# Kernel tuning notes

Hardware: AMD Instinct MI355X
Metric: run time of the kernel (lower is better)

Reference implementation:

```python
import jax, jax.numpy as jnp
import numpy as np

NUM_EXPERTS = 8
TOP_K = 2


def setup_inputs() -> dict:
    key = jax.random.key(0)
    ks = jax.random.split(key, 6)
    D, H, E = 1024, 4096, NUM_EXPERTS
    B, S = 4, 2048
    s = 0.02
    return {
        "x": jax.random.normal(ks[0], (B, S, D), jnp.float32),
        "scale_embeddings": jax.random.normal(ks[1], (10, D), jnp.float32) * s,
        "router_w": jax.random.normal(ks[2], (E, D), jnp.float32) * s,
        "router_b": jnp.zeros((E,), jnp.float32),
        "fc1_w": jax.random.normal(ks[3], (E, H, D), jnp.float32) * s,
        "fc1_b": jnp.zeros((E, H), jnp.float32),
        "fc2_w": jax.random.normal(ks[4], (E, D, H), jnp.float32) * s,
        "fc2_b": jnp.zeros((E, D), jnp.float32),
        "scale_idx": 3,
    }


def reference(x, scale_embeddings, router_w, router_b, fc1_w, fc1_b, fc2_w, fc2_b, scale_idx):
    B, S, D = x.shape
    T = B * S
    # Scale-aware router (eval mode: no jitter, temperature=1.0).
    xs = x + scale_embeddings[scale_idx][None, None, :]
    logits = jnp.einsum('bsd,ed->bse', xs, router_w) + router_b  # [B,S,E]
    top_w, top_idx = jax.lax.top_k(logits, TOP_K)                 # [B,S,K]
    top_w = jax.nn.softmax(top_w, axis=-1)

    # Dense per-expert FFN (tanh-approx GELU), then gather top-k expert outputs.
    xf = x.reshape(T, D)
    outs = []
    for e in range(NUM_EXPERTS):
        h = jax.nn.gelu(xf @ fc1_w[e].T + fc1_b[e], approximate=True)  # [T,H]
        outs.append(h @ fc2_w[e].T + fc2_b[e])                          # [T,D]
    all_out = jnp.stack(outs)                                           # [E,T,D]

    idx_f = top_idx.reshape(T, TOP_K)
    w_f = top_w.reshape(T, TOP_K)
    gathered = all_out[idx_f, jnp.arange(T)[:, None]]  # [T,K,D]
    out = (gathered * w_f[..., None]).sum(axis=1)      # [T,D]
    return out.reshape(B, S, D)
```

## Files before the change

### kernel.cpp

```cpp
#include <hip/hip_runtime.h>
#include <math.h>

#define TTOK 8192
#define DDIM 1024
#define HDIM 4096
#define NEXP 8
#define NASSIGN (TTOK * 2)

typedef float f32x4 __attribute__((ext_vector_type(4)));
typedef short s16x8 __attribute__((ext_vector_type(8)));

__device__ __forceinline__ unsigned short f2bf(float f) {
  union { float f; unsigned int u; } v; v.f = f;
  unsigned int u = v.u;
  u += 0x7FFFu + ((u >> 16) & 1u);
  return (unsigned short)(u >> 16);
}

__device__ __forceinline__ float gelu_fast(float x) {
  float u = 0.7978845608028654f * x * (1.0f + 0.044715f * x * x);
  return x / (1.0f + __expf(-2.0f * u));
}

__global__ void cvt_bf16_k(const float* __restrict__ w1, unsigned short* __restrict__ w1b,
                           const float* __restrict__ w2, unsigned short* __restrict__ w2b,
                           int n8) {
  int i = blockIdx.x * blockDim.x + threadIdx.x;
  const float* src; unsigned short* dst;
  if (i < n8) { src = w1; dst = w1b; } else { src = w2; dst = w2b; i -= n8; }
#pragma unroll
  for (int c = 0; c < 2; ++c) {
    float4 v = ((const float4*)src)[i * 2 + c];
    ushort4 o;
    o.x = f2bf(v.x); o.y = f2bf(v.y); o.z = f2bf(v.z); o.w = f2bf(v.w);
    ((ushort4*)dst)[i * 2 + c] = o;
  }
}

__global__ void router_k(const float* __restrict__ x, const float* __restrict__ se,
                         const int* __restrict__ sidx, const float* __restrict__ rw,
                         const float* __restrict__ rb,
                         int* __restrict__ e0, int* __restrict__ e1,
                         float* __restrict__ w0, float* __restrict__ w1,
                         int* __restrict__ counts) {
  int t = blockIdx.x * 4 + (threadIdx.x >> 6);
  int lane = threadIdx.x & 63;
  const float4* xp = (const float4*)(x + (size_t)t * DDIM) + lane * 4;
  const float4* sp = (const float4*)(se + (size_t)sidx[0] * DDIM) + lane * 4;
  float xs[16];
#pragma unroll
  for (int c = 0; c < 4; ++c) {
    float4 a = xp[c], b = sp[c];
    xs[c * 4 + 0] = a.x + b.x; xs[c * 4 + 1] = a.y + b.y;
    xs[c * 4 + 2] = a.z + b.z; xs[c * 4 + 3] = a.w + b.w;
  }
  double acc[NEXP];
#pragma unroll
  for (int e = 0; e < NEXP; ++e) acc[e] = 0.0;
#pragma unroll
  for (int e = 0; e < NEXP; ++e) {
    const float4* wp = (const float4*)(rw + (size_t)e * DDIM) + lane * 4;
#pragma unroll
    for (int c = 0; c < 4; ++c) {
      float4 wv = wp[c];
      acc[e] += (double)xs[c * 4 + 0] * wv.x + (double)xs[c * 4 + 1] * wv.y +
                (double)xs[c * 4 + 2] * wv.z + (double)xs[c * 4 + 3] * wv.w;
    }
  }
#pragma unroll
  for (int e = 0; e < NEXP; ++e) {
#pragma unroll
    for (int m = 32; m >= 1; m >>= 1) acc[e] += __shfl_xor(acc[e], m, 64);
  }
  if (lane == 0) {
    float lg[NEXP];
    for (int e = 0; e < NEXP; ++e) lg[e] = (float)acc[e] + rb[e];
    int i0 = 0; float l0 = lg[0];
    for (int e = 1; e < NEXP; ++e) if (lg[e] > l0) { l0 = lg[e]; i0 = e; }
    int i1 = -1; float l1 = -1e30f;
    for (int e = 0; e < NEXP; ++e) if (e != i0 && lg[e] > l1) { l1 = lg[e]; i1 = e; }
    float z = expf(l1 - l0);
    float p0 = 1.0f / (1.0f + z);
    e0[t] = i0; e1[t] = i1; w0[t] = p0; w1[t] = 1.0f - p0;
    atomicAdd(&counts[i0], 1);
    atomicAdd(&counts[i1], 1);
  }
}

__global__ void scan_k(const int* __restrict__ counts, int* __restrict__ offsets,
                       int* __restrict__ cursors, int4* __restrict__ tileT,
                       int* __restrict__ ntiles) {
  if (threadIdx.x == 0 && blockIdx.x == 0) {
    int s = 0;
    for (int e = 0; e < NEXP; ++e) { offsets[e] = s; cursors[e] = s; s += counts[e]; }
    offsets[NEXP] = s;
    int nt = 0;
    for (int e = 0; e < NEXP; ++e)
      for (int m0 = offsets[e]; m0 < offsets[e + 1]; m0 += 128)
        tileT[nt++] = make_int4(m0, offsets[e + 1], e, 0);
    ntiles[0] = nt;
  }
}

__global__ void scatter_k(const int* __restrict__ e0, const int* __restrict__ e1,
                          const float* __restrict__ w0, const float* __restrict__ w1,
                          int* __restrict__ cursors, int* __restrict__ buckets,
                          float* __restrict__ wts, int* __restrict__ s0,
                          int* __restrict__ s1) {
  int t = blockIdx.x * blockDim.x + threadIdx.x;
  if (t >= TTOK) return;
  int a = e0[t];
  int p = atomicAdd(&cursors[a], 1);
  buckets[p] = t; wts[p] = w0[t]; s0[t] = p;
  a = e1[t];
  p = atomicAdd(&cursors[a], 1);
  buckets[p] = t; wts[p] = w1[t]; s1[t] = p;
}

__global__ void gather_k(const float* __restrict__ x, const int* __restrict__ buckets,
                         unsigned short* __restrict__ Xg) {
  int r = blockIdx.x;
  int t = buckets[r];
  int i = threadIdx.x;
  float4 v = ((const float4*)(x + (size_t)t * DDIM))[i];
  ushort4 o;
  o.x = f2bf(v.x); o.y = f2bf(v.y); o.z = f2bf(v.z); o.w = f2bf(v.w);
  ((ushort4*)(Xg + (size_t)r * DDIM))[i] = o;
}

template <int KD, int ND, int EPI>
__global__ __launch_bounds__(256) void moe_gemm_k(
    const unsigned short* __restrict__ A,
    const unsigned short* __restrict__ W,
    const float* __restrict__ bias,
    const int4* __restrict__ tileT, const int* __restrict__ ntiles,
    unsigned short* __restrict__ Hout, float* __restrict__ Yout) {
  constexpr int NT = ND / 128;
  constexpr int G = NT / 8;
  __shared__ unsigned short As[128 * 64];
  __shared__ unsigned short Bs[128 * 64];

  const int tid = threadIdx.x;
  const int lane = tid & 63;
  const int w = tid >> 6;
  const int q = lane >> 4;
  const int c16 = lane & 15;
  const int cx = lane & 7;
  const int wrow = (w >> 1) * 64;
  const int wcol = (w & 1) * 64;
  const int srow = w * 8 + (lane >> 3);
  const int swz = (lane & 7) ^ (lane >> 3);

  const int xcd = blockIdx.x & 7;
  const int lid = blockIdx.x >> 3;
  const int bound = ntiles[0] * G;

  for (int idx = lid; idx < bound; idx += 256) {
    const int mt = idx / G;
    const int nb = xcd * G + (idx - mt * G);
    const int4 tl = tileT[mt];
    const int m0 = tl.x, row1 = tl.y, e = tl.z;
    const int n0 = nb * 128;
    const unsigned short* We = W + (size_t)e * ND * KD;

    const unsigned short* aptr[4];
    const unsigned short* bptr[4];
#pragma unroll
    for (int i = 0; i < 4; ++i) {
      int ar = m0 + i * 32 + srow;
      if (ar > row1 - 1) ar = row1 - 1;
      aptr[i] = A + (size_t)ar * KD + swz * 8;
      bptr[i] = We + (size_t)(n0 + i * 32 + srow) * KD + swz * 8;
    }

    f32x4 acc[4][4];
#pragma unroll
    for (int i = 0; i < 4; ++i)
#pragma unroll
      for (int j = 0; j < 4; ++j) acc[i][j] = {0.f, 0.f, 0.f, 0.f};

    for (int kt = 0; kt < KD / 64; ++kt) {
      const int k0 = kt * 64;
      __syncthreads();
#pragma unroll
      for (int i = 0; i < 4; ++i)
        __builtin_amdgcn_global_load_lds(
            (const __attribute__((address_space(1))) void*)(aptr[i] + k0),
            (__attribute__((address_space(3))) void*)(As + (i * 32 + w * 8) * 64),
            16, 0, 0);
#pragma unroll
      for (int i = 0; i < 4; ++i)
        __builtin_amdgcn_global_load_lds(
            (const __attribute__((address_space(1))) void*)(bptr[i] + k0),
            (__attribute__((address_space(3))) void*)(Bs + (i * 32 + w * 8) * 64),
            16, 0, 0);
      __syncthreads();
#pragma unroll
      for (int ks = 0; ks < 2; ++ks) {
        s16x8 af[4], bfr[4];
#pragma unroll
        for (int i = 0; i < 4; ++i)
          af[i] = *((const s16x8*)(As + (wrow + i * 16 + c16) * 64 +
                                   (((ks * 4 + q) ^ cx) * 8)));
#pragma unroll
        for (int j = 0; j < 4; ++j)
          bfr[j] = *((const s16x8*)(Bs + (wcol + j * 16 + c16) * 64 +
                                    (((ks * 4 + q) ^ cx) * 8)));
#pragma unroll
        for (int i = 0; i < 4; ++i)
#pragma unroll
          for (int j = 0; j < 4; ++j)
            acc[i][j] = __builtin_amdgcn_mfma_f32_16x16x32_bf16(af[i], bfr[j], acc[i][j], 0, 0, 0);
      }
    }

    float bj[4];
#pragma unroll
    for (int j = 0; j < 4; ++j)
      bj[j] = bias[(size_t)e * ND + n0 + wcol + j * 16 + c16];
#pragma unroll
    for (int i = 0; i < 4; ++i) {
#pragma unroll
      for (int r = 0; r < 4; ++r) {
        const int m = m0 + wrow + i * 16 + q * 4 + r;
        if (m < row1) {
          if (EPI == 0) {
#pragma unroll
            for (int j = 0; j < 4; ++j) {
              const int n = n0 + wcol + j * 16 + c16;
              Hout[(size_t)m * ND + n] = f2bf(gelu_fast(acc[i][j][r] + bj[j]));
            }
          } else {
#pragma unroll
            for (int j = 0; j < 4; ++j) {
              const int n = n0 + wcol + j * 16 + c16;
              Yout[(size_t)m * ND + n] = acc[i][j][r] + bj[j];
            }
          }
        }
      }
    }
  }
}

__global__ void combine_k(const float* __restrict__ Yr, const int* __restrict__ s0,
                          const int* __restrict__ s1, const float* __restrict__ wts,
                          float* __restrict__ out) {
  int t = blockIdx.x;
  int i = threadIdx.x;
  int a = s0[t], b = s1[t];
  float wa = wts[a], wb = wts[b];
  float4 va = ((const float4*)(Yr + (size_t)a * DDIM))[i];
  float4 vb = ((const float4*)(Yr + (size_t)b * DDIM))[i];
  float4 o;
  o.x = wa * va.x + wb * vb.x;
  o.y = wa * va.y + wb * vb.y;
  o.z = wa * va.z + wb * vb.z;
  o.w = wa * va.w + wb * vb.w;
  ((float4*)(out + (size_t)t * DDIM))[i] = o;
}

extern "C" void kernel_launch(void* const* d_in, const int* in_sizes, int n_in,
                              void* d_out, int out_size, void* d_ws, size_t ws_size,
                              hipStream_t stream) {
  const float* x  = (const float*)d_in[0];
  const float* se = (const float*)d_in[1];
  const float* rw = (const float*)d_in[2];
  const float* rb = (const float*)d_in[3];
  const float* w1 = (const float*)d_in[4];
  const float* b1 = (const float*)d_in[5];
  const float* w2 = (const float*)d_in[6];
  const float* b2 = (const float*)d_in[7];
  const int* sidx = (const int*)d_in[8];
  float* out = (float*)d_out;

  char* ws = (char*)d_ws;
  size_t off = 0;
  unsigned short* w1b = (unsigned short*)(ws + off); off += (size_t)NEXP * HDIM * DDIM * 2;
  unsigned short* w2b = (unsigned short*)(ws + off); off += (size_t)NEXP * DDIM * HDIM * 2;
  unsigned short* Xg  = (unsigned short*)(ws + off); off += (size_t)NASSIGN * DDIM * 2;
  unsigned short* Hb  = (unsigned short*)(ws + off); off += (size_t)NASSIGN * HDIM * 2;
  float* Yr = (float*)w1b;
  int*   counts  = (int*)(ws + off); off += 64;
  int*   offsets = (int*)(ws + off); off += 64;
  int*   cursors = (int*)(ws + off); off += 64;
  int*   ntiles  = (int*)(ws + off); off += 64;
  int*   e0  = (int*)(ws + off);   off += (size_t)TTOK * 4;
  int*   e1  = (int*)(ws + off);   off += (size_t)TTOK * 4;
  float* tw0 = (float*)(ws + off); off += (size_t)TTOK * 4;
  float* tw1 = (float*)(ws + off); off += (size_t)TTOK * 4;
  int*   s0  = (int*)(ws + off);   off += (size_t)TTOK * 4;
  int*   s1  = (int*)(ws + off);   off += (size_t)TTOK * 4;
  int*   buckets = (int*)(ws + off); off += (size_t)NASSIGN * 4;
  float* wts = (float*)(ws + off);   off += (size_t)NASSIGN * 4;
  int4*  tileT = (int4*)(ws + off);  off += 256 * 16;

  hipMemsetAsync(counts, 0, 64, stream);

  const int n8 = NEXP * HDIM * DDIM / 8;
  cvt_bf16_k<<<2 * n8 / 256, 256, 0, stream>>>(w1, w1b, w2, w2b, n8);
  router_k<<<TTOK / 4, 256, 0, stream>>>(x, se, sidx, rw, rb, e0, e1, tw0, tw1, counts);
  scan_k<<<1, 64, 0, stream>>>(counts, offsets, cursors, tileT, ntiles);
  scatter_k<<<TTOK / 256, 256, 0, stream>>>(e0, e1, tw0, tw1, cursors, buckets, wts, s0, s1);
  gather_k<<<NASSIGN, 256, 0, stream>>>(x, buckets, Xg);

  moe_gemm_k<DDIM, HDIM, 0><<<2048, 256, 0, stream>>>(Xg, w1b, b1, tileT, ntiles, Hb, Yr);
  moe_gemm_k<HDIM, DDIM, 1><<<2048, 256, 0, stream>>>(Hb, w2b, b2, tileT, ntiles, Hb, Yr);
  combine_k<<<TTOK, 256, 0, stream>>>(Yr, s0, s1, wts, out);
}
```

Measured before the change: 1.145 ms.

## Double-buffer MoE GEMM LDS tiles and fuse scatter with token gather

The GEMM main loop switches from single-buffered 64-wide K tiles, with two barriers per step, to double-buffered 32-wide K tiles. The next stage's global-to-LDS loads are issued before the current stage is computed, with one barrier per step. The scatter and gather kernels are merged into one per-token kernel that converts x once and writes it to both assigned slots. The combine kernel now reads per-token weights directly, with wider per-thread work. Smaller K stages mean more loop iterations and barriers, and the overlap depends on how the compiler schedules the LDS-DMA waits.

```diff
diff --git a/kernel.cpp b/kernel.cpp
--- a/kernel.cpp
+++ b/kernel.cpp
@@ -15,6 +15,15 @@
   unsigned int u = v.u;
   u += 0x7FFFu + ((u >> 16) & 1u);
   return (unsigned short)(u >> 16);
+}
+
+__device__ __forceinline__ s16x8 f2bf8(float4 a, float4 b) {
+  s16x8 o;
+  o[0] = (short)f2bf(a.x); o[1] = (short)f2bf(a.y);
+  o[2] = (short)f2bf(a.z); o[3] = (short)f2bf(a.w);
+  o[4] = (short)f2bf(b.x); o[5] = (short)f2bf(b.y);
+  o[6] = (short)f2bf(b.z); o[7] = (short)f2bf(b.w);
+  return o;
 }
 
 __device__ __forceinline__ float gelu_fast(float x) {
@@ -28,13 +37,9 @@
   int i = blockIdx.x * blockDim.x + threadIdx.x;
   const float* src; unsigned short* dst;
   if (i < n8) { src = w1; dst = w1b; } else { src = w2; dst = w2b; i -= n8; }
-#pragma unroll
-  for (int c = 0; c < 2; ++c) {
-    float4 v = ((const float4*)src)[i * 2 + c];
-    ushort4 o;
-    o.x = f2bf(v.x); o.y = f2bf(v.y); o.z = f2bf(v.z); o.w = f2bf(v.w);
-    ((ushort4*)dst)[i * 2 + c] = o;
-  }
+  float4 a = ((const float4*)src)[2 * i];
+  float4 b = ((const float4*)src)[2 * i + 1];
+  ((s16x8*)dst)[i] = f2bf8(a, b);
 }
 
 __global__ void router_k(const float* __restrict__ x, const float* __restrict__ se,
@@ -102,30 +107,25 @@
   }
 }
 
-__global__ void scatter_k(const int* __restrict__ e0, const int* __restrict__ e1,
-                          const float* __restrict__ w0, const float* __restrict__ w1,
-                          int* __restrict__ cursors, int* __restrict__ buckets,
-                          float* __restrict__ wts, int* __restrict__ s0,
-                          int* __restrict__ s1) {
-  int t = blockIdx.x * blockDim.x + threadIdx.x;
-  if (t >= TTOK) return;
-  int a = e0[t];
-  int p = atomicAdd(&cursors[a], 1);
-  buckets[p] = t; wts[p] = w0[t]; s0[t] = p;
-  a = e1[t];
-  p = atomicAdd(&cursors[a], 1);
-  buckets[p] = t; wts[p] = w1[t]; s1[t] = p;
-}
-
-__global__ void gather_k(const float* __restrict__ x, const int* __restrict__ buckets,
-                         unsigned short* __restrict__ Xg) {
-  int r = blockIdx.x;
-  int t = buckets[r];
-  int i = threadIdx.x;
-  float4 v = ((const float4*)(x + (size_t)t * DDIM))[i];
-  ushort4 o;
-  o.x = f2bf(v.x); o.y = f2bf(v.y); o.z = f2bf(v.z); o.w = f2bf(v.w);
-  ((ushort4*)(Xg + (size_t)r * DDIM))[i] = o;
+__global__ void sg_k(const float* __restrict__ x, const int* __restrict__ e0,
+                     const int* __restrict__ e1, int* __restrict__ cursors,
+                     int* __restrict__ s0, int* __restrict__ s1,
+                     unsigned short* __restrict__ Xg) {
+  __shared__ int sp0, sp1;
+  const int t = blockIdx.x;
+  const int i = threadIdx.x;
+  if (i == 0) {
+    int p = atomicAdd(&cursors[e0[t]], 1);
+    sp0 = p; s0[t] = p;
+    p = atomicAdd(&cursors[e1[t]], 1);
+    sp1 = p; s1[t] = p;
+  }
+  float4 a = ((const float4*)(x + (size_t)t * DDIM))[2 * i];
+  float4 b = ((const float4*)(x + (size_t)t * DDIM))[2 * i + 1];
+  s16x8 o = f2bf8(a, b);
+  __syncthreads();
+  ((s16x8*)(Xg + (size_t)sp0 * DDIM))[i] = o;
+  ((s16x8*)(Xg + (size_t)sp1 * DDIM))[i] = o;
 }
 
 template <int KD, int ND, int EPI>
@@ -137,19 +137,20 @@
     unsigned short* __restrict__ Hout, float* __restrict__ Yout) {
   constexpr int NT = ND / 128;
   constexpr int G = NT / 8;
-  __shared__ unsigned short As[128 * 64];
-  __shared__ unsigned short Bs[128 * 64];
+  constexpr int NK = KD / 32;
+  __shared__ unsigned short As[2][128 * 32];
+  __shared__ unsigned short Bs[2][128 * 32];
 
   const int tid = threadIdx.x;
   const int lane = tid & 63;
   const int w = tid >> 6;
   const int q = lane >> 4;
   const int c16 = lane & 15;
-  const int cx = lane & 7;
+  const int cxx = c16 & 3;
   const int wrow = (w >> 1) * 64;
   const int wcol = (w & 1) * 64;
-  const int srow = w * 8 + (lane >> 3);
-  const int swz = (lane & 7) ^ (lane >> 3);
+  const int grow = tid >> 2;
+  const int gchunk = (tid & 3) ^ (grow & 3);
 
   const int xcd = blockIdx.x & 7;
   const int lid = blockIdx.x >> 3;
@@ -163,14 +164,14 @@
     const int n0 = nb * 128;
     const unsigned short* We = W + (size_t)e * ND * KD;
 
-    const unsigned short* aptr[4];
-    const unsigned short* bptr[4];
-#pragma unroll
-    for (int i = 0; i < 4; ++i) {
-      int ar = m0 + i * 32 + srow;
+    const unsigned short* aptr[2];
+    const unsigned short* bptr[2];
+#pragma unroll
+    for (int ig = 0; ig < 2; ++ig) {
+      int ar = m0 + ig * 64 + grow;
       if (ar > row1 - 1) ar = row1 - 1;
-      aptr[i] = A + (size_t)ar * KD + swz * 8;
-      bptr[i] = We + (size_t)(n0 + i * 32 + srow) * KD + swz * 8;
+      aptr[ig] = A + (size_t)ar * KD + gchunk * 8;
+      bptr[ig] = We + (size_t)(n0 + ig * 64 + grow) * KD + gchunk * 8;
     }
 
     f32x4 acc[4][4];
@@ -179,40 +180,43 @@
 #pragma unroll
       for (int j = 0; j < 4; ++j) acc[i][j] = {0.f, 0.f, 0.f, 0.f};
 
-    for (int kt = 0; kt < KD / 64; ++kt) {
-      const int k0 = kt * 64;
+    __syncthreads();
+
+#define LOAD_STAGE(buf, k0)                                                        \
+    {                                                                              \
+      _Pragma("unroll")                                                            \
+      for (int ig = 0; ig < 2; ++ig) {                                             \
+        __builtin_amdgcn_global_load_lds(                                          \
+            (const __attribute__((address_space(1))) void*)(aptr[ig] + (k0)),      \
+            (__attribute__((address_space(3))) void*)(&As[buf][(ig * 64 + w * 16) * 32]), \
+            16, 0, 0);                                                             \
+        __builtin_amdgcn_global_load_lds(                                          \
+            (const __attribute__((address_space(1))) void*)(bptr[ig] + (k0)),      \
+            (__attribute__((address_space(3))) void*)(&Bs[buf][(ig * 64 + w * 16) * 32]), \
+            16, 0, 0);                                                             \
+      }                                                                            \
+    }
+
+    LOAD_STAGE(0, 0);
+
+    for (int kt = 0; kt < NK; ++kt) {
       __syncthreads();
+      if (kt + 1 < NK) LOAD_STAGE((kt + 1) & 1, (kt + 1) * 32);
+      const int buf = kt & 1;
+      s16x8 af[4], bv[4];
 #pragma unroll
       for (int i = 0; i < 4; ++i)
-        __builtin_amdgcn_global_load_lds(
-            (const __attribute__((address_space(1))) void*)(aptr[i] + k0),
-            (__attribute__((address_space(3))) void*)(As + (i * 32 + w * 8) * 64),
-            16, 0, 0);
+        af[i] = *((const s16x8*)(&As[buf][(wrow + i * 16 + c16) * 32 + (q ^ cxx) * 8]));
+#pragma unroll
+      for (int j = 0; j < 4; ++j)
+        bv[j] = *((const s16x8*)(&Bs[buf][(wcol + j * 16 + c16) * 32 + (q ^ cxx) * 8]));
 #pragma unroll
       for (int i = 0; i < 4; ++i)
-        __builtin_amdgcn_global_load_lds(
-            (const __attribute__((address_space(1))) void*)(bptr[i] + k0),
-            (__attribute__((address_space(3))) void*)(Bs + (i * 32 + w * 8) * 64),
-            16, 0, 0);
-      __syncthreads();
-#pragma unroll
-      for (int ks = 0; ks < 2; ++ks) {
-        s16x8 af[4], bfr[4];
-#pragma unroll
-        for (int i = 0; i < 4; ++i)
-          af[i] = *((const s16x8*)(As + (wrow + i * 16 + c16) * 64 +
-                                   (((ks * 4 + q) ^ cx) * 8)));
 #pragma unroll
         for (int j = 0; j < 4; ++j)
-          bfr[j] = *((const s16x8*)(Bs + (wcol + j * 16 + c16) * 64 +
-                                    (((ks * 4 + q) ^ cx) * 8)));
-#pragma unroll
-        for (int i = 0; i < 4; ++i)
-#pragma unroll
-          for (int j = 0; j < 4; ++j)
-            acc[i][j] = __builtin_amdgcn_mfma_f32_16x16x32_bf16(af[i], bfr[j], acc[i][j], 0, 0, 0);
-      }
-    }
+          acc[i][j] = __builtin_amdgcn_mfma_f32_16x16x32_bf16(af[i], bv[j], acc[i][j], 0, 0, 0);
+    }
+#undef LOAD_STAGE
 
     float bj[4];
 #pragma unroll
@@ -244,20 +248,25 @@
 }
 
 __global__ void combine_k(const float* __restrict__ Yr, const int* __restrict__ s0,
-                          const int* __restrict__ s1, const float* __restrict__ wts,
-                          float* __restrict__ out) {
-  int t = blockIdx.x;
-  int i = threadIdx.x;
-  int a = s0[t], b = s1[t];
-  float wa = wts[a], wb = wts[b];
-  float4 va = ((const float4*)(Yr + (size_t)a * DDIM))[i];
-  float4 vb = ((const float4*)(Yr + (size_t)b * DDIM))[i];
-  float4 o;
-  o.x = wa * va.x + wb * vb.x;
-  o.y = wa * va.y + wb * vb.y;
-  o.z = wa * va.z + wb * vb.z;
-  o.w = wa * va.w + wb * vb.w;
-  ((float4*)(out + (size_t)t * DDIM))[i] = o;
+                          const int* __restrict__ s1, const float* __restrict__ tw0,
+                          const float* __restrict__ tw1, float* __restrict__ out) {
+  const int t = blockIdx.x;
+  const int i = threadIdx.x;
+  const int a = s0[t], b = s1[t];
+  const float wa = tw0[t], wb = tw1[t];
+  const float4* pa = (const float4*)(Yr + (size_t)a * DDIM);
+  const float4* pb = (const float4*)(Yr + (size_t)b * DDIM);
+  float4* po = (float4*)(out + (size_t)t * DDIM);
+#pragma unroll
+  for (int c = 0; c < 2; ++c) {
+    float4 va = pa[2 * i + c], vb = pb[2 * i + c];
+    float4 o;
+    o.x = wa * va.x + wb * vb.x;
+    o.y = wa * va.y + wb * vb.y;
+    o.z = wa * va.z + wb * vb.z;
+    o.w = wa * va.w + wb * vb.w;
+    po[2 * i + c] = o;
+  }
 }
 
 extern "C" void kernel_launch(void* const* d_in, const int* in_sizes, int n_in,
@@ -291,8 +300,6 @@
   float* tw1 = (float*)(ws + off); off += (size_t)TTOK * 4;
   int*   s0  = (int*)(ws + off);   off += (size_t)TTOK * 4;
   int*   s1  = (int*)(ws + off);   off += (size_t)TTOK * 4;
-  int*   buckets = (int*)(ws + off); off += (size_t)NASSIGN * 4;
-  float* wts = (float*)(ws + off);   off += (size_t)NASSIGN * 4;
   int4*  tileT = (int4*)(ws + off);  off += 256 * 16;
 
   hipMemsetAsync(counts, 0, 64, stream);
@@ -301,10 +308,9 @@
   cvt_bf16_k<<<2 * n8 / 256, 256, 0, stream>>>(w1, w1b, w2, w2b, n8);
   router_k<<<TTOK / 4, 256, 0, stream>>>(x, se, sidx, rw, rb, e0, e1, tw0, tw1, counts);
   scan_k<<<1, 64, 0, stream>>>(counts, offsets, cursors, tileT, ntiles);
-  scatter_k<<<TTOK / 256, 256, 0, stream>>>(e0, e1, tw0, tw1, cursors, buckets, wts, s0, s1);
-  gather_k<<<NASSIGN, 256, 0, stream>>>(x, buckets, Xg);
+  sg_k<<<TTOK, 128, 0, stream>>>(x, e0, e1, cursors, s0, s1, Xg);
 
   moe_gemm_k<DDIM, HDIM, 0><<<2048, 256, 0, stream>>>(Xg, w1b, b1, tileT, ntiles, Hb, Yr);
   moe_gemm_k<HDIM, DDIM, 1><<<2048, 256, 0, stream>>>(Hb, w2b, b2, tileT, ntiles, Hb, Yr);
-  combine_k<<<TTOK, 256, 0, stream>>>(Yr, s0, s1, wts, out);
-}
+  combine_k<<<TTOK, 128, 0, stream>>>(Yr, s0, s1, tw0, tw1, out);
+}
```

Result: slower. 1.235 ms (+7.9%).
